# Performance work log

Measured on AMD Instinct MI355X. Metric: run time of the kernel, lower is better.

Reference implementation:

```python
import jax, jax.numpy as jnp
import numpy as np


def _feature_map(x):
    # elu(x) + 1, the canonical positive feature map for linear attention
    return jax.nn.elu(x) + 1.0


def setup_inputs() -> dict:
    key = jax.random.key(0)
    kq, kk, kv = jax.random.split(key, 3)
    B, T, H, D, M = 2, 2048, 8, 64, 64
    q = jax.random.normal(kq, (B, T, H, D), dtype=jnp.float32)
    k = jax.random.normal(kk, (B, T, H, D), dtype=jnp.float32)
    v = jax.random.normal(kv, (B, T, H, M), dtype=jnp.float32)
    return {"q": q, "k": k, "v": v}


def reference(q, k, v):
    # q,k: [B,T,H,D]; v: [B,T,H,M]
    qf = _feature_map(q)
    kf = _feature_map(k)
    # running sum of keys over time (causal)
    k_sum = jnp.cumsum(kf, axis=1)                      # [B,T,H,D]
    z = 1.0 / jnp.einsum('bthd,bthd->bth', qf, k_sum)   # [B,T,H]
    # outer products k_i v_i^T; NOTE: original torch code cumsums over dim=-2
    # (the D axis of the [B,T,H,D,M] tensor), reproduced faithfully here.
    kv = jnp.einsum('bthd,bthm->bthdm', kf, v)           # [B,T,H,D,M]
    kv_sum = jnp.cumsum(kv, axis=-2)                     # cumsum over D, per source
    out = jnp.einsum('bthd,bthdm,bth->bthm', qf, kv_sum, z)
    return out
```

## Files before the change

kernel.cpp:

```cpp
#include <hip/hip_runtime.h>
#include <hip/hip_bf16.h>

#define BB 2
#define TT 2048
#define HH 8
#define DD 64
#define CC 256
#define TC (TT / CC)
#define STRIDE (HH * DD)
#define NBH (BB * HH)
#define PW (CC / 16)

__device__ __forceinline__ float feat(float x) {
    return x > 0.f ? x + 1.f : __expf(x);
}


__global__ void __launch_bounds__(64)
chunk_sums_kernel(const float* __restrict__ k, float* __restrict__ ws) {
    const int idx  = blockIdx.x;
    const int c    = idx & (CC - 1);
    const int h    = (idx >> 8) & (HH - 1);
    const int b    = idx >> 11;
    const int lane = threadIdx.x;
    const int g    = lane & 15;
    const int seg  = lane >> 4;

    const size_t off0 = (((size_t)b * TT + c * TC + seg) * HH + h) * DD + g * 4;
    const float4 k0 = *(const float4*)(k + off0);
    const float4 k1 = *(const float4*)(k + off0 + (size_t)4 * STRIDE);

    float4 s;
    s.x = feat(k0.x) + feat(k1.x);
    s.y = feat(k0.y) + feat(k1.y);
    s.z = feat(k0.z) + feat(k1.z);
    s.w = feat(k0.w) + feat(k1.w);

    s.x += __shfl_xor(s.x, 16, 64); s.y += __shfl_xor(s.y, 16, 64);
    s.z += __shfl_xor(s.z, 16, 64); s.w += __shfl_xor(s.w, 16, 64);
    s.x += __shfl_xor(s.x, 32, 64); s.y += __shfl_xor(s.y, 32, 64);
    s.z += __shfl_xor(s.z, 32, 64); s.w += __shfl_xor(s.w, 32, 64);

    if (seg == 0)
        *(float4*)(ws + (size_t)idx * DD + g * 4) = s;
}

__global__ void __launch_bounds__(1024)
prefix_kernel(float* __restrict__ ws) {
    const int bh   = blockIdx.x;
    const int lane = threadIdx.x & 63;
    const int w    = threadIdx.x >> 6;

    size_t base = ((size_t)bh * CC + w * PW) * DD + lane;

    float val[PW];
    #pragma unroll
    for (int i = 0; i < PW; ++i) val[i] = ws[base + (size_t)i * DD];

    float run = 0.f, excl[PW];
    #pragma unroll
    for (int i = 0; i < PW; ++i) { excl[i] = run; run += val[i]; }

    __shared__ float tot[16][DD];
    tot[w][lane] = run;
    __syncthreads();

    float carry = 0.f;
    for (int w2 = 0; w2 < w; ++w2) carry += tot[w2][lane];

    #pragma unroll
    for (int i = 0; i < PW; ++i) ws[base + (size_t)i * DD] = excl[i] + carry;
}

__global__ void __launch_bounds__(64)
linattn_kernel(const float* __restrict__ q, const float* __restrict__ k,
               const float* __restrict__ v, const float* __restrict__ ws,
               float* __restrict__ out) {
    const int idx  = blockIdx.x;
    const int c    = idx & (CC - 1);
    const int h    = (idx >> 8) & (HH - 1);
    const int b    = idx >> 11;
    const int lane = threadIdx.x;
    const int g    = lane & 15;
    const int seg  = lane >> 4;

    const size_t off0 = (((size_t)b * TT + c * TC + seg) * HH + h) * DD + g * 4;
    const size_t off1 = off0 + (size_t)4 * STRIDE;

    float4 kf0 = *(const float4*)(k + off0);
    float4 kf1 = *(const float4*)(k + off1);
    float4 qf0 = *(const float4*)(q + off0);
    float4 qf1 = *(const float4*)(q + off1);
    const float4 vv0 = *(const float4*)(v + off0);
    const float4 vv1 = *(const float4*)(v + off1);
    const float4 carry = *(const float4*)(ws + (size_t)idx * DD + g * 4);

    kf0.x = feat(kf0.x); kf0.y = feat(kf0.y); kf0.z = feat(kf0.z); kf0.w = feat(kf0.w);
    kf1.x = feat(kf1.x); kf1.y = feat(kf1.y); kf1.z = feat(kf1.z); kf1.w = feat(kf1.w);
    qf0.x = feat(qf0.x); qf0.y = feat(qf0.y); qf0.z = feat(qf0.z); qf0.w = feat(qf0.w);
    qf1.x = feat(qf1.x); qf1.y = feat(qf1.y); qf1.z = feat(qf1.z); qf1.w = feat(qf1.w);

    float4 i0 = kf0, i1 = kf1;
    {
        float u;
        u = __shfl_up(i0.x, 16, 64); if (seg >= 1) i0.x += u;
        u = __shfl_up(i0.y, 16, 64); if (seg >= 1) i0.y += u;
        u = __shfl_up(i0.z, 16, 64); if (seg >= 1) i0.z += u;
        u = __shfl_up(i0.w, 16, 64); if (seg >= 1) i0.w += u;
        u = __shfl_up(i1.x, 16, 64); if (seg >= 1) i1.x += u;
        u = __shfl_up(i1.y, 16, 64); if (seg >= 1) i1.y += u;
        u = __shfl_up(i1.z, 16, 64); if (seg >= 1) i1.z += u;
        u = __shfl_up(i1.w, 16, 64); if (seg >= 1) i1.w += u;
        u = __shfl_up(i0.x, 32, 64); if (seg >= 2) i0.x += u;
        u = __shfl_up(i0.y, 32, 64); if (seg >= 2) i0.y += u;
        u = __shfl_up(i0.z, 32, 64); if (seg >= 2) i0.z += u;
        u = __shfl_up(i0.w, 32, 64); if (seg >= 2) i0.w += u;
        u = __shfl_up(i1.x, 32, 64); if (seg >= 2) i1.x += u;
        u = __shfl_up(i1.y, 32, 64); if (seg >= 2) i1.y += u;
        u = __shfl_up(i1.z, 32, 64); if (seg >= 2) i1.z += u;
        u = __shfl_up(i1.w, 32, 64); if (seg >= 2) i1.w += u;
    }
    float4 S0;
    S0.x = __shfl(i0.x, 48 + g, 64);
    S0.y = __shfl(i0.y, 48 + g, 64);
    S0.z = __shfl(i0.z, 48 + g, 64);
    S0.w = __shfl(i0.w, 48 + g, 64);

    float4 run0, run1;
    run0.x = carry.x + i0.x; run0.y = carry.y + i0.y;
    run0.z = carry.z + i0.z; run0.w = carry.w + i0.w;
    run1.x = carry.x + S0.x + i1.x; run1.y = carry.y + S0.y + i1.y;
    run1.z = carry.z + S0.z + i1.z; run1.w = carry.w + S0.w + i1.w;

    float4 p0, p1;
    p0.x = kf0.x; p0.y = p0.x + kf0.y; p0.z = p0.y + kf0.z; p0.w = p0.z + kf0.w;
    p1.x = kf1.x; p1.y = p1.x + kf1.y; p1.z = p1.y + kf1.z; p1.w = p1.z + kf1.w;
    float c0 = p0.w, c1 = p1.w;
    #pragma unroll
    for (int o = 1; o <= 8; o <<= 1) {
        float u0 = __shfl_up(c0, o, 16);
        float u1 = __shfl_up(c1, o, 16);
        if (g >= o) { c0 += u0; c1 += u1; }
    }
    const float e0 = c0 - p0.w;
    const float e1 = c1 - p1.w;
    float4 pre0, pre1;
    pre0.x = p0.x + e0; pre0.y = p0.y + e0; pre0.z = p0.z + e0; pre0.w = p0.w + e0;
    pre1.x = p1.x + e1; pre1.y = p1.y + e1; pre1.z = p1.z + e1; pre1.w = p1.w + e1;

    float s1_0 = qf0.x * pre0.x + qf0.y * pre0.y + qf0.z * pre0.z + qf0.w * pre0.w;
    float s2_0 = qf0.x * run0.x + qf0.y * run0.y + qf0.z * run0.z + qf0.w * run0.w;
    float s1_1 = qf1.x * pre1.x + qf1.y * pre1.y + qf1.z * pre1.z + qf1.w * pre1.w;
    float s2_1 = qf1.x * run1.x + qf1.y * run1.y + qf1.z * run1.z + qf1.w * run1.w;
    #pragma unroll
    for (int o = 1; o <= 8; o <<= 1) {
        s1_0 += __shfl_xor(s1_0, o, 64);
        s2_0 += __shfl_xor(s2_0, o, 64);
        s1_1 += __shfl_xor(s1_1, o, 64);
        s2_1 += __shfl_xor(s2_1, o, 64);
    }

    const float r0 = s1_0 * __builtin_amdgcn_rcpf(s2_0);
    const float r1 = s1_1 * __builtin_amdgcn_rcpf(s2_1);
    float4 o0, o1;
    o0.x = vv0.x * r0; o0.y = vv0.y * r0; o0.z = vv0.z * r0; o0.w = vv0.w * r0;
    o1.x = vv1.x * r1; o1.y = vv1.y * r1; o1.z = vv1.z * r1; o1.w = vv1.w * r1;
    *(float4*)(out + off0) = o0;
    *(float4*)(out + off1) = o1;
}

extern "C" void kernel_launch(void* const* d_in, const int* in_sizes, int n_in,
                              void* d_out, int out_size, void* d_ws, size_t ws_size,
                              hipStream_t stream) {
    const float* q = (const float*)d_in[0];
    const float* k = (const float*)d_in[1];
    const float* v = (const float*)d_in[2];
    float* out = (float*)d_out;
    float* ws  = (float*)d_ws;

    const int nblk = BB * HH * CC;
    chunk_sums_kernel<<<nblk, 64, 0, stream>>>(k, ws);
    prefix_kernel<<<NBH, 1024, 0, stream>>>(ws);
    linattn_kernel<<<nblk, 64, 0, stream>>>(q, k, v, ws, out);
}
```

Before: 78.24 us.

## Drop prefix kernel; compute chunk carries inline with fewer, larger chunks

Removes the separate prefix-scan launch. Each linattn block now sums the preceding chunk totals from the workspace itself, with 4 lanes strided over prior chunks followed by a cross-lane reduction. The chunk count is halved to 128, so each block handles 16 timesteps (4 per lane group) and the per-block redundant carry summation stays bounded. This trades one kernel launch and a global round trip for redundant O(c) reads per block, which rise to about 32 float4 loads per lane for the last chunks.

```diff
diff --git a/kernel.cpp b/kernel.cpp
--- a/kernel.cpp
+++ b/kernel.cpp
@@ -1,18 +1,40 @@
 #include <hip/hip_runtime.h>
-#include <hip/hip_bf16.h>
 
 #define BB 2
 #define TT 2048
 #define HH 8
 #define DD 64
-#define CC 256
+#define CC 128
 #define TC (TT / CC)
+#define NI 4
 #define STRIDE (HH * DD)
 #define NBH (BB * HH)
-#define PW (CC / 16)
 
 __device__ __forceinline__ float feat(float x) {
     return x > 0.f ? x + 1.f : __expf(x);
+}
+
+__device__ __forceinline__ void feat4(float4& a) {
+    a.x = feat(a.x); a.y = feat(a.y); a.z = feat(a.z); a.w = feat(a.w);
+}
+
+__device__ __forceinline__ void segscan(float4& a, int seg) {
+    float u;
+    u = __shfl_up(a.x, 16, 64); if (seg >= 1) a.x += u;
+    u = __shfl_up(a.y, 16, 64); if (seg >= 1) a.y += u;
+    u = __shfl_up(a.z, 16, 64); if (seg >= 1) a.z += u;
+    u = __shfl_up(a.w, 16, 64); if (seg >= 1) a.w += u;
+    u = __shfl_up(a.x, 32, 64); if (seg >= 2) a.x += u;
+    u = __shfl_up(a.y, 32, 64); if (seg >= 2) a.y += u;
+    u = __shfl_up(a.z, 32, 64); if (seg >= 2) a.z += u;
+    u = __shfl_up(a.w, 32, 64); if (seg >= 2) a.w += u;
+}
+
+__device__ __forceinline__ void xorred4(float4& a) {
+    a.x += __shfl_xor(a.x, 16, 64); a.y += __shfl_xor(a.y, 16, 64);
+    a.z += __shfl_xor(a.z, 16, 64); a.w += __shfl_xor(a.w, 16, 64);
+    a.x += __shfl_xor(a.x, 32, 64); a.y += __shfl_xor(a.y, 32, 64);
+    a.z += __shfl_xor(a.z, 32, 64); a.w += __shfl_xor(a.w, 32, 64);
 }
 
 
@@ -20,56 +42,22 @@
 chunk_sums_kernel(const float* __restrict__ k, float* __restrict__ ws) {
     const int idx  = blockIdx.x;
     const int c    = idx & (CC - 1);
-    const int h    = (idx >> 8) & (HH - 1);
-    const int b    = idx >> 11;
+    const int h    = (idx >> 7) & (HH - 1);
+    const int b    = idx >> 10;
     const int lane = threadIdx.x;
     const int g    = lane & 15;
     const int seg  = lane >> 4;
 
     const size_t off0 = (((size_t)b * TT + c * TC + seg) * HH + h) * DD + g * 4;
-    const float4 k0 = *(const float4*)(k + off0);
-    const float4 k1 = *(const float4*)(k + off0 + (size_t)4 * STRIDE);
-
-    float4 s;
-    s.x = feat(k0.x) + feat(k1.x);
-    s.y = feat(k0.y) + feat(k1.y);
-    s.z = feat(k0.z) + feat(k1.z);
-    s.w = feat(k0.w) + feat(k1.w);
-
-    s.x += __shfl_xor(s.x, 16, 64); s.y += __shfl_xor(s.y, 16, 64);
-    s.z += __shfl_xor(s.z, 16, 64); s.w += __shfl_xor(s.w, 16, 64);
-    s.x += __shfl_xor(s.x, 32, 64); s.y += __shfl_xor(s.y, 32, 64);
-    s.z += __shfl_xor(s.z, 32, 64); s.w += __shfl_xor(s.w, 32, 64);
-
+    float4 s = make_float4(0.f, 0.f, 0.f, 0.f);
+    #pragma unroll
+    for (int i = 0; i < NI; ++i) {
+        const float4 kv = *(const float4*)(k + off0 + (size_t)(4 * i) * STRIDE);
+        s.x += feat(kv.x); s.y += feat(kv.y); s.z += feat(kv.z); s.w += feat(kv.w);
+    }
+    xorred4(s);
     if (seg == 0)
         *(float4*)(ws + (size_t)idx * DD + g * 4) = s;
-}
-
-__global__ void __launch_bounds__(1024)
-prefix_kernel(float* __restrict__ ws) {
-    const int bh   = blockIdx.x;
-    const int lane = threadIdx.x & 63;
-    const int w    = threadIdx.x >> 6;
-
-    size_t base = ((size_t)bh * CC + w * PW) * DD + lane;
-
-    float val[PW];
-    #pragma unroll
-    for (int i = 0; i < PW; ++i) val[i] = ws[base + (size_t)i * DD];
-
-    float run = 0.f, excl[PW];
-    #pragma unroll
-    for (int i = 0; i < PW; ++i) { excl[i] = run; run += val[i]; }
-
-    __shared__ float tot[16][DD];
-    tot[w][lane] = run;
-    __syncthreads();
-
-    float carry = 0.f;
-    for (int w2 = 0; w2 < w; ++w2) carry += tot[w2][lane];
-
-    #pragma unroll
-    for (int i = 0; i < PW; ++i) ws[base + (size_t)i * DD] = excl[i] + carry;
 }
 
 __global__ void __launch_bounds__(64)
@@ -78,95 +66,75 @@
                float* __restrict__ out) {
     const int idx  = blockIdx.x;
     const int c    = idx & (CC - 1);
-    const int h    = (idx >> 8) & (HH - 1);
-    const int b    = idx >> 11;
+    const int h    = (idx >> 7) & (HH - 1);
+    const int b    = idx >> 10;
     const int lane = threadIdx.x;
     const int g    = lane & 15;
     const int seg  = lane >> 4;
 
     const size_t off0 = (((size_t)b * TT + c * TC + seg) * HH + h) * DD + g * 4;
-    const size_t off1 = off0 + (size_t)4 * STRIDE;
 
-    float4 kf0 = *(const float4*)(k + off0);
-    float4 kf1 = *(const float4*)(k + off1);
-    float4 qf0 = *(const float4*)(q + off0);
-    float4 qf1 = *(const float4*)(q + off1);
-    const float4 vv0 = *(const float4*)(v + off0);
-    const float4 vv1 = *(const float4*)(v + off1);
-    const float4 carry = *(const float4*)(ws + (size_t)idx * DD + g * 4);
-
-    kf0.x = feat(kf0.x); kf0.y = feat(kf0.y); kf0.z = feat(kf0.z); kf0.w = feat(kf0.w);
-    kf1.x = feat(kf1.x); kf1.y = feat(kf1.y); kf1.z = feat(kf1.z); kf1.w = feat(kf1.w);
-    qf0.x = feat(qf0.x); qf0.y = feat(qf0.y); qf0.z = feat(qf0.z); qf0.w = feat(qf0.w);
-    qf1.x = feat(qf1.x); qf1.y = feat(qf1.y); qf1.z = feat(qf1.z); qf1.w = feat(qf1.w);
-
-    float4 i0 = kf0, i1 = kf1;
-    {
-        float u;
-        u = __shfl_up(i0.x, 16, 64); if (seg >= 1) i0.x += u;
-        u = __shfl_up(i0.y, 16, 64); if (seg >= 1) i0.y += u;
-        u = __shfl_up(i0.z, 16, 64); if (seg >= 1) i0.z += u;
-        u = __shfl_up(i0.w, 16, 64); if (seg >= 1) i0.w += u;
-        u = __shfl_up(i1.x, 16, 64); if (seg >= 1) i1.x += u;
-        u = __shfl_up(i1.y, 16, 64); if (seg >= 1) i1.y += u;
-        u = __shfl_up(i1.z, 16, 64); if (seg >= 1) i1.z += u;
-        u = __shfl_up(i1.w, 16, 64); if (seg >= 1) i1.w += u;
-        u = __shfl_up(i0.x, 32, 64); if (seg >= 2) i0.x += u;
-        u = __shfl_up(i0.y, 32, 64); if (seg >= 2) i0.y += u;
-        u = __shfl_up(i0.z, 32, 64); if (seg >= 2) i0.z += u;
-        u = __shfl_up(i0.w, 32, 64); if (seg >= 2) i0.w += u;
-        u = __shfl_up(i1.x, 32, 64); if (seg >= 2) i1.x += u;
-        u = __shfl_up(i1.y, 32, 64); if (seg >= 2) i1.y += u;
-        u = __shfl_up(i1.z, 32, 64); if (seg >= 2) i1.z += u;
-        u = __shfl_up(i1.w, 32, 64); if (seg >= 2) i1.w += u;
-    }
-    float4 S0;
-    S0.x = __shfl(i0.x, 48 + g, 64);
-    S0.y = __shfl(i0.y, 48 + g, 64);
-    S0.z = __shfl(i0.z, 48 + g, 64);
-    S0.w = __shfl(i0.w, 48 + g, 64);
-
-    float4 run0, run1;
-    run0.x = carry.x + i0.x; run0.y = carry.y + i0.y;
-    run0.z = carry.z + i0.z; run0.w = carry.w + i0.w;
-    run1.x = carry.x + S0.x + i1.x; run1.y = carry.y + S0.y + i1.y;
-    run1.z = carry.z + S0.z + i1.z; run1.w = carry.w + S0.w + i1.w;
-
-    float4 p0, p1;
-    p0.x = kf0.x; p0.y = p0.x + kf0.y; p0.z = p0.y + kf0.z; p0.w = p0.z + kf0.w;
-    p1.x = kf1.x; p1.y = p1.x + kf1.y; p1.z = p1.y + kf1.z; p1.w = p1.z + kf1.w;
-    float c0 = p0.w, c1 = p1.w;
+    float4 kf[NI], qf[NI], vv[NI];
     #pragma unroll
-    for (int o = 1; o <= 8; o <<= 1) {
-        float u0 = __shfl_up(c0, o, 16);
-        float u1 = __shfl_up(c1, o, 16);
-        if (g >= o) { c0 += u0; c1 += u1; }
-    }
-    const float e0 = c0 - p0.w;
-    const float e1 = c1 - p1.w;
-    float4 pre0, pre1;
-    pre0.x = p0.x + e0; pre0.y = p0.y + e0; pre0.z = p0.z + e0; pre0.w = p0.w + e0;
-    pre1.x = p1.x + e1; pre1.y = p1.y + e1; pre1.z = p1.z + e1; pre1.w = p1.w + e1;
-
-    float s1_0 = qf0.x * pre0.x + qf0.y * pre0.y + qf0.z * pre0.z + qf0.w * pre0.w;
-    float s2_0 = qf0.x * run0.x + qf0.y * run0.y + qf0.z * run0.z + qf0.w * run0.w;
-    float s1_1 = qf1.x * pre1.x + qf1.y * pre1.y + qf1.z * pre1.z + qf1.w * pre1.w;
-    float s2_1 = qf1.x * run1.x + qf1.y * run1.y + qf1.z * run1.z + qf1.w * run1.w;
-    #pragma unroll
-    for (int o = 1; o <= 8; o <<= 1) {
-        s1_0 += __shfl_xor(s1_0, o, 64);
-        s2_0 += __shfl_xor(s2_0, o, 64);
-        s1_1 += __shfl_xor(s1_1, o, 64);
-        s2_1 += __shfl_xor(s2_1, o, 64);
+    for (int i = 0; i < NI; ++i) {
+        const size_t o = off0 + (size_t)(4 * i) * STRIDE;
+        kf[i] = *(const float4*)(k + o);
+        qf[i] = *(const float4*)(q + o);
+        vv[i] = *(const float4*)(v + o);
     }
 
-    const float r0 = s1_0 * __builtin_amdgcn_rcpf(s2_0);
-    const float r1 = s1_1 * __builtin_amdgcn_rcpf(s2_1);
-    float4 o0, o1;
-    o0.x = vv0.x * r0; o0.y = vv0.y * r0; o0.z = vv0.z * r0; o0.w = vv0.w * r0;
-    o1.x = vv1.x * r1; o1.y = vv1.y * r1; o1.z = vv1.z * r1; o1.w = vv1.w * r1;
-    *(float4*)(out + off0) = o0;
-    *(float4*)(out + off1) = o1;
+    const float* wsg = ws + (size_t)(idx - c) * DD + g * 4;
+    float4 carry = make_float4(0.f, 0.f, 0.f, 0.f);
+    for (int cp = seg; cp < c; cp += 4) {
+        const float4 t = *(const float4*)(wsg + (size_t)cp * DD);
+        carry.x += t.x; carry.y += t.y; carry.z += t.z; carry.w += t.w;
+    }
+    xorred4(carry);
+
+    #pragma unroll
+    for (int i = 0; i < NI; ++i) { feat4(kf[i]); feat4(qf[i]); }
+
+    float4 base = carry;
+    #pragma unroll
+    for (int i = 0; i < NI; ++i) {
+        float4 inc = kf[i];
+        segscan(inc, seg);
+        float4 run;
+        run.x = base.x + inc.x; run.y = base.y + inc.y;
+        run.z = base.z + inc.z; run.w = base.w + inc.w;
+        if (i < NI - 1) {
+            base.x += __shfl(inc.x, 48 + g, 64);
+            base.y += __shfl(inc.y, 48 + g, 64);
+            base.z += __shfl(inc.z, 48 + g, 64);
+            base.w += __shfl(inc.w, 48 + g, 64);
+        }
+
+        float4 p;
+        p.x = kf[i].x; p.y = p.x + kf[i].y; p.z = p.y + kf[i].z; p.w = p.z + kf[i].w;
+        float cg = p.w;
+        #pragma unroll
+        for (int o = 1; o <= 8; o <<= 1) {
+            const float u = __shfl_up(cg, o, 16);
+            if (g >= o) cg += u;
+        }
+        const float e  = cg - p.w;
+        const float sq = qf[i].x + qf[i].y + qf[i].z + qf[i].w;
+        float s1 = qf[i].x * p.x + qf[i].y * p.y + qf[i].z * p.z + qf[i].w * p.w
+                 + e * sq;
+        float s2 = qf[i].x * run.x + qf[i].y * run.y + qf[i].z * run.z
+                 + qf[i].w * run.w;
+        #pragma unroll
+        for (int o = 1; o <= 8; o <<= 1) {
+            s1 += __shfl_xor(s1, o, 64);
+            s2 += __shfl_xor(s2, o, 64);
+        }
+
+        const float r = s1 * __builtin_amdgcn_rcpf(s2);
+        float4 ov;
+        ov.x = vv[i].x * r; ov.y = vv[i].y * r;
+        ov.z = vv[i].z * r; ov.w = vv[i].w * r;
+        *(float4*)(out + off0 + (size_t)(4 * i) * STRIDE) = ov;
+    }
 }
 
 extern "C" void kernel_launch(void* const* d_in, const int* in_sizes, int n_in,
@@ -180,6 +148,5 @@
 
     const int nblk = BB * HH * CC;
     chunk_sums_kernel<<<nblk, 64, 0, stream>>>(k, ws);
-    prefix_kernel<<<NBH, 1024, 0, stream>>>(ws);
     linattn_kernel<<<nblk, 64, 0, stream>>>(q, k, v, ws, out);
 }
```

New measurement: 86.55 us. 1.11x slower.

## Drop prefix kernel; each block sums preceding chunk totals itself

Applied to the files above, without the earlier changes.

Removes the separate cross-chunk prefix-scan launch. Each linattn block now loops over all earlier chunk sums for its (b,h) and reduces them across its four lane groups with shuffles, so it computes its own carry. This trades one kernel launch and its dependency barrier for redundant reads, up to 255 float4 per lane group in the last chunks, which mostly hit cache. It also factors the per-lane offset out of the s1 dot product using the sum of q.

```diff
diff --git a/kernel.cpp b/kernel.cpp
--- a/kernel.cpp
+++ b/kernel.cpp
@@ -1,5 +1,4 @@
 #include <hip/hip_runtime.h>
-#include <hip/hip_bf16.h>
 
 #define BB 2
 #define TT 2048
@@ -9,7 +8,6 @@
 #define TC (TT / CC)
 #define STRIDE (HH * DD)
 #define NBH (BB * HH)
-#define PW (CC / 16)
 
 __device__ __forceinline__ float feat(float x) {
     return x > 0.f ? x + 1.f : __expf(x);
@@ -45,33 +43,6 @@
         *(float4*)(ws + (size_t)idx * DD + g * 4) = s;
 }
 
-__global__ void __launch_bounds__(1024)
-prefix_kernel(float* __restrict__ ws) {
-    const int bh   = blockIdx.x;
-    const int lane = threadIdx.x & 63;
-    const int w    = threadIdx.x >> 6;
-
-    size_t base = ((size_t)bh * CC + w * PW) * DD + lane;
-
-    float val[PW];
-    #pragma unroll
-    for (int i = 0; i < PW; ++i) val[i] = ws[base + (size_t)i * DD];
-
-    float run = 0.f, excl[PW];
-    #pragma unroll
-    for (int i = 0; i < PW; ++i) { excl[i] = run; run += val[i]; }
-
-    __shared__ float tot[16][DD];
-    tot[w][lane] = run;
-    __syncthreads();
-
-    float carry = 0.f;
-    for (int w2 = 0; w2 < w; ++w2) carry += tot[w2][lane];
-
-    #pragma unroll
-    for (int i = 0; i < PW; ++i) ws[base + (size_t)i * DD] = excl[i] + carry;
-}
-
 __global__ void __launch_bounds__(64)
 linattn_kernel(const float* __restrict__ q, const float* __restrict__ k,
                const float* __restrict__ v, const float* __restrict__ ws,
@@ -93,7 +64,17 @@
     float4 qf1 = *(const float4*)(q + off1);
     const float4 vv0 = *(const float4*)(v + off0);
     const float4 vv1 = *(const float4*)(v + off1);
-    const float4 carry = *(const float4*)(ws + (size_t)idx * DD + g * 4);
+
+    const float* wsg = ws + (size_t)(idx - c) * DD + g * 4;
+    float4 carry = make_float4(0.f, 0.f, 0.f, 0.f);
+    for (int cp = seg; cp < c; cp += 4) {
+        const float4 t = *(const float4*)(wsg + (size_t)cp * DD);
+        carry.x += t.x; carry.y += t.y; carry.z += t.z; carry.w += t.w;
+    }
+    carry.x += __shfl_xor(carry.x, 16, 64); carry.y += __shfl_xor(carry.y, 16, 64);
+    carry.z += __shfl_xor(carry.z, 16, 64); carry.w += __shfl_xor(carry.w, 16, 64);
+    carry.x += __shfl_xor(carry.x, 32, 64); carry.y += __shfl_xor(carry.y, 32, 64);
+    carry.z += __shfl_xor(carry.z, 32, 64); carry.w += __shfl_xor(carry.w, 32, 64);
 
     kf0.x = feat(kf0.x); kf0.y = feat(kf0.y); kf0.z = feat(kf0.z); kf0.w = feat(kf0.w);
     kf1.x = feat(kf1.x); kf1.y = feat(kf1.y); kf1.z = feat(kf1.z); kf1.w = feat(kf1.w);
@@ -144,13 +125,12 @@
     }
     const float e0 = c0 - p0.w;
     const float e1 = c1 - p1.w;
-    float4 pre0, pre1;
-    pre0.x = p0.x + e0; pre0.y = p0.y + e0; pre0.z = p0.z + e0; pre0.w = p0.w + e0;
-    pre1.x = p1.x + e1; pre1.y = p1.y + e1; pre1.z = p1.z + e1; pre1.w = p1.w + e1;
 
-    float s1_0 = qf0.x * pre0.x + qf0.y * pre0.y + qf0.z * pre0.z + qf0.w * pre0.w;
+    const float sq0 = qf0.x + qf0.y + qf0.z + qf0.w;
+    const float sq1 = qf1.x + qf1.y + qf1.z + qf1.w;
+    float s1_0 = qf0.x * p0.x + qf0.y * p0.y + qf0.z * p0.z + qf0.w * p0.w + e0 * sq0;
     float s2_0 = qf0.x * run0.x + qf0.y * run0.y + qf0.z * run0.z + qf0.w * run0.w;
-    float s1_1 = qf1.x * pre1.x + qf1.y * pre1.y + qf1.z * pre1.z + qf1.w * pre1.w;
+    float s1_1 = qf1.x * p1.x + qf1.y * p1.y + qf1.z * p1.z + qf1.w * p1.w + e1 * sq1;
     float s2_1 = qf1.x * run1.x + qf1.y * run1.y + qf1.z * run1.z + qf1.w * run1.w;
     #pragma unroll
     for (int o = 1; o <= 8; o <<= 1) {
@@ -180,6 +160,5 @@
 
     const int nblk = BB * HH * CC;
     chunk_sums_kernel<<<nblk, 64, 0, stream>>>(k, ws);
-    prefix_kernel<<<NBH, 1024, 0, stream>>>(ws);
     linattn_kernel<<<nblk, 64, 0, stream>>>(q, k, v, ws, out);
 }
```

After: 92.62 us. 1.18x slower.
